# Kernel tuning notes

Hardware: AMD Instinct MI355X
Metric: run time of the kernel (lower is better)

The kernel has to match this reference:

```python
import jax, jax.numpy as jnp
import numpy as np

K, D, N, W, OUT = 16, 2, 16384, 256, 1
TW = 0.2  # fixed_transition_width


def setup_inputs() -> dict:
    key = jax.random.key(0)
    ks = jax.random.split(key, 9)
    # 4x4 grid of subdomains over [0,1]^2
    edges = np.linspace(0.0, 1.0, 5).astype(np.float32)
    mins = np.array([[edges[i], edges[j]] for i in range(4) for j in range(4)], np.float32)
    maxs = mins + 0.25

    def init_w(k, shape, fan_in):
        return jax.random.normal(k, shape, jnp.float32) / np.sqrt(fan_in).astype(np.float32)

    return {
        "x": jax.random.uniform(ks[0], (N, D), jnp.float32),
        "W0": init_w(ks[1], (K, D, W), D),
        "b0": jnp.zeros((K, W), jnp.float32),
        "W1": init_w(ks[2], (K, W, W), W),
        "b1": jnp.zeros((K, W), jnp.float32),
        "W2": init_w(ks[3], (K, W, W), W),
        "b2": jnp.zeros((K, W), jnp.float32),
        "W3": init_w(ks[4], (K, W, OUT), W),
        "b3": jnp.zeros((K, OUT), jnp.float32),
        "xmins": jnp.asarray(mins),
        "xmaxs": jnp.asarray(maxs),
    }


def _cosine_window(xmins, xmaxs, wmin, x):
    """Normalized cosine partition-of-unity weights. x:[N,D], xmins/xmaxs:[K,D] -> [N,K]."""
    # smooth ramp 0->1 over [xmin-w, xmin+w] and 1->0 over [xmax-w, xmax+w], per dim
    t_l = jnp.clip((x[None] - (xmins - wmin)[:, None]) / (2.0 * wmin), 0.0, 1.0)  # [K,N,D]
    t_r = jnp.clip(((xmaxs + wmin)[:, None] - x[None]) / (2.0 * wmin), 0.0, 1.0)
    w_raw = jnp.prod(0.25 * (1.0 - jnp.cos(jnp.pi * t_l)) * (1.0 - jnp.cos(jnp.pi * t_r)), axis=-1)  # [K,N]
    w = w_raw / (jnp.sum(w_raw, axis=0, keepdims=True) + 1e-9)
    return w.T  # [N,K]


def reference(x, W0, b0, W1, b1, W2, b2, W3, b3, xmins, xmaxs):
    all_w = _cosine_window(xmins, xmaxs, TW, x)  # [N,K]
    # per-subdomain normalization of x to [-1,1]
    center = (xmins + xmaxs) * 0.5
    scale = jnp.maximum((xmaxs - xmins) * 0.5, 1e-9)
    xn = (x[None] - center[:, None]) / scale[:, None]  # [K,N,D]
    # batched small MLPs (one per subdomain), tanh hidden activations
    h = jnp.tanh(jnp.einsum('knd,kdw->knw', xn, W0) + b0[:, None])
    h = jnp.tanh(jnp.einsum('knw,kwv->knv', h, W1) + b1[:, None])
    h = jnp.tanh(jnp.einsum('knw,kwv->knv', h, W2) + b2[:, None])
    sub = jnp.einsum('knw,kwo->kno', h, W3) + b3[:, None]  # [K,N,OUT]
    # window-weighted combine; ansatz is identity in the NN output
    return jnp.einsum('nk,kno->no', all_w, sub)  # [N,OUT]
```

## Files before the change

### kernel.cpp

```cpp
#include <hip/hip_runtime.h>
#include <stdint.h>

#define TWF 0.2f
#define NPTS 16384

typedef __attribute__((ext_vector_type(8))) short short8;
typedef __attribute__((ext_vector_type(4))) float floatx4;

__device__ __forceinline__ short f2bf(float f){
  unsigned u = __float_as_uint(f);
  u += 0x7fff + ((u >> 16) & 1);
  return (short)(u >> 16);
}
__device__ __forceinline__ float bf2f(short s){
  return __uint_as_float(((unsigned)(unsigned short)s) << 16);
}
__device__ __forceinline__ float fast_tanh(float x){
  float e = __builtin_amdgcn_exp2f(x * 2.885390082f);
  float r = __builtin_amdgcn_rcpf(e + 1.f);
  return fmaf(-2.f, r, 1.f);
}
__device__ __forceinline__ float cospi_t(float t){
  return __builtin_amdgcn_cosf(t * 0.5f);
}
__device__ __forceinline__ unsigned cvt_pk_bf16(float lo, float hi){
  unsigned r;
  asm("v_cvt_pk_bf16_f32 %0, %1, %2" : "=v"(r) : "v"(lo), "v"(hi));
  return r;
}

#define WS_W      0
#define WS_CNT    (4u<<20)
#define WS_ILIST  ((4u<<20) + 4096u)
#define WS_WLIST  ((5u<<20) + 4096u)
#define CNT(k)    counts[(k) * 32]

__global__ __launch_bounds__(256) void prep_fused(
    const float* __restrict__ W1, const float* __restrict__ W2,
    const float* __restrict__ x,  const float* __restrict__ xmins,
    const float* __restrict__ xmaxs, short* __restrict__ dst,
    int* __restrict__ counts, int* __restrict__ ilist, float* __restrict__ wlist,
    float* __restrict__ out){
  if (blockIdx.x < 1024){
    int gid = blockIdx.x * 256 + threadIdx.x;
    int lane = gid & 63; int rest = gid >> 6;
    int jt = rest & 15; rest >>= 4;
    int ks = rest & 7;  rest >>= 3;
    int k  = rest & 15; int mat = rest >> 4;
    const float* W = mat ? W2 : W1;
    int j   = jt * 16 + (lane & 15);
    int kk0 = ks * 32 + (lane >> 4) * 8;
    short8 v;
    #pragma unroll
    for (int jj = 0; jj < 8; jj++)
      v[jj] = f2bf(W[k * 65536 + (kk0 + jj) * 256 + j]);
    *(short8*)(dst + (size_t)gid * 8) = v;
  } else {
    __shared__ int s_wcnt[4];
    __shared__ int s_base;
    int b2    = blockIdx.x - 1024;
    int g     = b2 & 3;
    int chunk = b2 >> 2;
    int t     = threadIdx.x;
    int gid   = chunk * 256 + t;
    int lane  = t & 63, wave = t >> 6;
    if (g == 0) out[gid] = 0.f;
    float px = x[gid * 2 + 0], py = x[gid * 2 + 1];
    float wr[16]; float sum = 0.f;
    #pragma unroll
    for (int k = 0; k < 16; k++){
      float w = 1.f;
      #pragma unroll
      for (int d = 0; d < 2; d++){
        float xv = d ? py : px;
        float mn = xmins[k * 2 + d], mx = xmaxs[k * 2 + d];
        float tl = fminf(fmaxf((xv - (mn - TWF)) * (1.f / (2.f * TWF)), 0.f), 1.f);
        float tr = fminf(fmaxf(((mx + TWF) - xv) * (1.f / (2.f * TWF)), 0.f), 1.f);
        w *= 0.25f * (1.f - cospi_t(tl)) * (1.f - cospi_t(tr));
      }
      wr[k] = w; sum += w;
    }
    float inv = 1.f / (sum + 1e-9f);
    #pragma unroll 1
    for (int kk = 0; kk < 4; kk++){
      int k = g * 4 + ((kk + chunk) & 3);
      bool act = wr[k] > 0.f;
      unsigned long long mask = __ballot(act);
      if (lane == 0) s_wcnt[wave] = (int)__popcll(mask);
      __syncthreads();
      int tot = s_wcnt[0] + s_wcnt[1] + s_wcnt[2] + s_wcnt[3];
      int wpre = 0;
      #pragma unroll
      for (int w = 0; w < 4; w++) wpre += (w < wave) ? s_wcnt[w] : 0;
      if (t == 0) s_base = atomicAdd(&CNT(k), tot);
      __syncthreads();
      if (act){
        int pos = s_base + wpre + (int)__popcll(mask & ((1ull << lane) - 1ull));
        ilist[k * NPTS + pos] = gid;
        wlist[k * NPTS + pos] = wr[k] * inv;
      }
    }
  }
}

__device__ __forceinline__ void store_h_packed(
    short* lds_h, const floatx4 (&acc)[4][4], const floatx4 (&bb)[4],
    int wave, int quad, int col){
  #pragma unroll
  for (int rt = 0; rt < 4; rt++){
    const int j0    = (wave * 4 + rt) * 16 + quad * 4;
    const int cbase = j0 >> 3;
    const int off   = j0 & 7;
    #pragma unroll
    for (int ct = 0; ct < 4; ct++){
      const int m = ct * 16 + col;
      float t0 = fast_tanh(acc[rt][ct][0] + bb[rt][0]);
      float t1 = fast_tanh(acc[rt][ct][1] + bb[rt][1]);
      float t2 = fast_tanh(acc[rt][ct][2] + bb[rt][2]);
      float t3 = fast_tanh(acc[rt][ct][3] + bb[rt][3]);
      uint2 v = make_uint2(cvt_pk_bf16(t0, t1), cvt_pk_bf16(t2, t3));
      *(uint2*)&lds_h[m * 256 + ((cbase ^ (m & 7)) << 3) + off] = v;
    }
  }
}

__global__ __launch_bounds__(256, 4) void fbpinn_main(
    const float* __restrict__ x,  const float* __restrict__ W0, const float* __restrict__ b0,
    const float* __restrict__ b1, const float* __restrict__ b2,
    const float* __restrict__ W3, const float* __restrict__ b3,
    const float* __restrict__ xmins, const float* __restrict__ xmaxs,
    const short* __restrict__ wsw, const int* __restrict__ counts,
    const int* __restrict__ ilist, const float* __restrict__ wlist,
    float* __restrict__ out)
{
  __shared__ short lds_h[64 * 256];
  __shared__ float s_xn[64 * 2];
  __shared__ float s_win[64];
  __shared__ int   s_pidx[64];
  __shared__ float s_w3[256];
  __shared__ float s_w0[512];

  const int t    = threadIdx.x;
  const int lane = t & 63;
  const int wave = t >> 6;
  const int col  = lane & 15;
  const int quad = lane >> 4;

  int tb[17]; tb[0] = 0;
  #pragma unroll
  for (int kk = 0; kk < 16; kk++) tb[kk + 1] = tb[kk] + ((CNT(kk) + 63) >> 6);
  const int total = tb[16];

  const int xcd   = blockIdx.x & 7;
  const int nb    = gridDim.x >> 3;
  const int chunk = (total + 7) >> 3;

  for (int idx = blockIdx.x >> 3; idx < chunk; idx += nb){
    const int tile = xcd * chunk + idx;
    if (tile >= total) break;
    int k = 0;
    #pragma unroll
    for (int kk = 1; kk < 16; kk++) k += (tile >= tb[kk]);
    const int base = (tile - tb[k]) * 64;
    const int cnt  = CNT(k);

    __syncthreads();

    s_w3[t] = W3[k * 256 + t];
    s_w0[t] = W0[k * 512 + t];
    s_w0[256 + t] = W0[k * 512 + 256 + t];
    if (t < 64){
      int gi = base + t;
      bool valid = gi < cnt;
      int pidx = valid ? ilist[k * NPTS + gi] : 0;
      float w  = valid ? wlist[k * NPTS + gi] : 0.f;
      s_pidx[t] = pidx;
      s_win[t]  = w;
      float px = x[pidx * 2 + 0], py = x[pidx * 2 + 1];
      float cx = (xmins[k * 2 + 0] + xmaxs[k * 2 + 0]) * 0.5f;
      float cy = (xmins[k * 2 + 1] + xmaxs[k * 2 + 1]) * 0.5f;
      float sx = fmaxf((xmaxs[k * 2 + 0] - xmins[k * 2 + 0]) * 0.5f, 1e-9f);
      float sy = fmaxf((xmaxs[k * 2 + 1] - xmins[k * 2 + 1]) * 0.5f, 1e-9f);
      s_xn[t * 2 + 0] = (px - cx) / sx;
      s_xn[t * 2 + 1] = (py - cy) / sy;
    }
    __syncthreads();

    {
      short8 wfr[4], xfr[4];
      #pragma unroll
      for (int rt = 0; rt < 4; rt++){
        int j = (wave * 4 + rt) * 16 + col;
        short8 a;
        #pragma unroll
        for (int i = 0; i < 8; i++) a[i] = 0;
        a[0] = (quad == 0) ? f2bf(s_w0[j])       : (short)0;
        a[1] = (quad == 0) ? f2bf(s_w0[256 + j]) : (short)0;
        wfr[rt] = a;
      }
      #pragma unroll
      for (int ct = 0; ct < 4; ct++){
        int m = ct * 16 + col;
        short8 b;
        #pragma unroll
        for (int i = 0; i < 8; i++) b[i] = 0;
        b[0] = (quad == 0) ? f2bf(s_xn[m * 2 + 0]) : (short)0;
        b[1] = (quad == 0) ? f2bf(s_xn[m * 2 + 1]) : (short)0;
        xfr[ct] = b;
      }
      floatx4 bb[4];
      #pragma unroll
      for (int rt = 0; rt < 4; rt++)
        bb[rt] = *(const floatx4*)&b0[k * 256 + (wave * 4 + rt) * 16 + quad * 4];
      floatx4 acc[4][4];
      #pragma unroll
      for (int a = 0; a < 4; a++)
        #pragma unroll
        for (int b = 0; b < 4; b++)
          acc[a][b] = (floatx4){0.f, 0.f, 0.f, 0.f};
      #pragma unroll
      for (int rt = 0; rt < 4; rt++)
        #pragma unroll
        for (int ct = 0; ct < 4; ct++)
          acc[rt][ct] = __builtin_amdgcn_mfma_f32_16x16x32_bf16(wfr[rt], xfr[ct], acc[rt][ct], 0, 0, 0);
      store_h_packed(lds_h, acc, bb, wave, quad, col);
      __syncthreads();
    }

    #pragma unroll 1
    for (int layer = 0; layer < 2; layer++){
      const short8* wb = (const short8*)(wsw + (size_t)layer * 1048576)
                         + ((size_t)(k * 8) * 16 + wave * 4) * 64 + lane;
      const float*  bp = layer ? b2 : b1;
      floatx4 bb[4];
      #pragma unroll
      for (int rt = 0; rt < 4; rt++)
        bb[rt] = *(const floatx4*)&bp[k * 256 + (wave * 4 + rt) * 16 + quad * 4];
      floatx4 acc[4][4];
      #pragma unroll
      for (int a = 0; a < 4; a++)
        #pragma unroll
        for (int b = 0; b < 4; b++)
          acc[a][b] = (floatx4){0.f, 0.f, 0.f, 0.f};

      short8 wcur[4];
      #pragma unroll
      for (int rt = 0; rt < 4; rt++) wcur[rt] = wb[rt * 64];

      #pragma unroll
      for (int ks = 0; ks < 8; ks++){
        short8 wnxt[4];
        if (ks < 7){
          #pragma unroll
          for (int rt = 0; rt < 4; rt++)
            wnxt[rt] = wb[(ks + 1) * 1024 + rt * 64];
        }
        short8 hfr[4];
        #pragma unroll
        for (int ct = 0; ct < 4; ct++){
          int m   = ct * 16 + col;
          int pos = (ks * 4 + quad) ^ (m & 7);
          hfr[ct] = *(const short8*)&lds_h[m * 256 + pos * 8];
        }
        #pragma unroll
        for (int rt = 0; rt < 4; rt++)
          #pragma unroll
          for (int ct = 0; ct < 4; ct++)
            acc[rt][ct] = __builtin_amdgcn_mfma_f32_16x16x32_bf16(wcur[rt], hfr[ct], acc[rt][ct], 0, 0, 0);
        if (ks < 7){
          #pragma unroll
          for (int rt = 0; rt < 4; rt++) wcur[rt] = wnxt[rt];
        }
      }
      __syncthreads();

      store_h_packed(lds_h, acc, bb, wave, quad, col);
      __syncthreads();
    }

    {
      int m = t >> 2, q = t & 3;
      float dot = 0.f;
      #pragma unroll
      for (int cc = 0; cc < 8; cc++){
        int ci  = q * 8 + cc;
        int pos = ci ^ (m & 7);
        short8 hv = *(const short8*)&lds_h[m * 256 + pos * 8];
        #pragma unroll
        for (int jj = 0; jj < 8; jj++)
          dot = fmaf(bf2f(hv[jj]), s_w3[ci * 8 + jj], dot);
      }
      dot += __shfl_xor(dot, 1);
      dot += __shfl_xor(dot, 2);
      if (q == 0 && s_win[m] != 0.f)
        atomicAdd(&out[s_pidx[m]], s_win[m] * (dot + b3[k]));
    }
  }
}

extern "C" void kernel_launch(void* const* d_in, const int* in_sizes, int n_in,
                              void* d_out, int out_size, void* d_ws, size_t ws_size,
                              hipStream_t stream){
  const float* x     = (const float*)d_in[0];
  const float* W0    = (const float*)d_in[1];
  const float* b0    = (const float*)d_in[2];
  const float* W1    = (const float*)d_in[3];
  const float* b1    = (const float*)d_in[4];
  const float* W2    = (const float*)d_in[5];
  const float* b2    = (const float*)d_in[6];
  const float* W3    = (const float*)d_in[7];
  const float* b3    = (const float*)d_in[8];
  const float* xmins = (const float*)d_in[9];
  const float* xmaxs = (const float*)d_in[10];
  float* out = (float*)d_out;

  char* ws = (char*)d_ws;
  short* wsw   = (short*)(ws + WS_W);
  int*   cnts  = (int*)  (ws + WS_CNT);
  int*   ilist = (int*)  (ws + WS_ILIST);
  float* wlist = (float*)(ws + WS_WLIST);

  (void)hipMemsetAsync(cnts, 0, 4096, stream);
  prep_fused<<<1024 + 256, 256, 0, stream>>>(W1, W2, x, xmins, xmaxs,
                                             wsw, cnts, ilist, wlist, out);
  fbpinn_main<<<2048, 256, 0, stream>>>(x, W0, b0, b1, b2, W3, b3, xmins, xmaxs,
                                        wsw, cnts, ilist, wlist, out);
}
```

Baseline: 139.1 us.

## Pack point records in prep and reorganize bucketing per subdomain block

The bucketing part of the prep kernel now assigns each block one subdomain and 1024 points. It writes a single packed float4 record holding normalized coordinates, the normalized window weight and the point index, and needs only one atomic per block. The main kernel reads that record instead of gathering ilist, wlist and x and recomputing the normalization, which removes a dependent gather. The main grid is also halved to 1024 blocks. In exchange, each prep block recomputes all 16 window weights for four points per thread, and the record buffer is twice as large as before.

```diff
diff --git a/kernel.cpp b/kernel.cpp
--- a/kernel.cpp
+++ b/kernel.cpp
@@ -30,16 +30,15 @@
 }
 
 #define WS_W      0
-#define WS_CNT    (4u<<20)
-#define WS_ILIST  ((4u<<20) + 4096u)
-#define WS_WLIST  ((5u<<20) + 4096u)
+#define WS_REC    (4u<<20)
+#define WS_CNT    (8u<<20)
 #define CNT(k)    counts[(k) * 32]
 
 __global__ __launch_bounds__(256) void prep_fused(
     const float* __restrict__ W1, const float* __restrict__ W2,
     const float* __restrict__ x,  const float* __restrict__ xmins,
     const float* __restrict__ xmaxs, short* __restrict__ dst,
-    int* __restrict__ counts, int* __restrict__ ilist, float* __restrict__ wlist,
+    int* __restrict__ counts, floatx4* __restrict__ rec,
     float* __restrict__ out){
   if (blockIdx.x < 1024){
     int gid = blockIdx.x * 256 + threadIdx.x;
@@ -56,49 +55,80 @@
       v[jj] = f2bf(W[k * 65536 + (kk0 + jj) * 256 + j]);
     *(short8*)(dst + (size_t)gid * 8) = v;
   } else {
-    __shared__ int s_wcnt[4];
+    __shared__ int s_wrt[4][4];
     __shared__ int s_base;
-    int b2    = blockIdx.x - 1024;
-    int g     = b2 & 3;
-    int chunk = b2 >> 2;
-    int t     = threadIdx.x;
-    int gid   = chunk * 256 + t;
-    int lane  = t & 63, wave = t >> 6;
-    if (g == 0) out[gid] = 0.f;
-    float px = x[gid * 2 + 0], py = x[gid * 2 + 1];
-    float wr[16]; float sum = 0.f;
-    #pragma unroll
-    for (int k = 0; k < 16; k++){
-      float w = 1.f;
-      #pragma unroll
-      for (int d = 0; d < 2; d++){
-        float xv = d ? py : px;
-        float mn = xmins[k * 2 + d], mx = xmaxs[k * 2 + d];
-        float tl = fminf(fmaxf((xv - (mn - TWF)) * (1.f / (2.f * TWF)), 0.f), 1.f);
-        float tr = fminf(fmaxf(((mx + TWF) - xv) * (1.f / (2.f * TWF)), 0.f), 1.f);
-        w *= 0.25f * (1.f - cospi_t(tl)) * (1.f - cospi_t(tr));
-      }
-      wr[k] = w; sum += w;
-    }
-    float inv = 1.f / (sum + 1e-9f);
-    #pragma unroll 1
-    for (int kk = 0; kk < 4; kk++){
-      int k = g * 4 + ((kk + chunk) & 3);
-      bool act = wr[k] > 0.f;
-      unsigned long long mask = __ballot(act);
-      if (lane == 0) s_wcnt[wave] = (int)__popcll(mask);
-      __syncthreads();
-      int tot = s_wcnt[0] + s_wcnt[1] + s_wcnt[2] + s_wcnt[3];
-      int wpre = 0;
-      #pragma unroll
-      for (int w = 0; w < 4; w++) wpre += (w < wave) ? s_wcnt[w] : 0;
-      if (t == 0) s_base = atomicAdd(&CNT(k), tot);
-      __syncthreads();
-      if (act){
-        int pos = s_base + wpre + (int)__popcll(mask & ((1ull << lane) - 1ull));
-        ilist[k * NPTS + pos] = gid;
-        wlist[k * NPTS + pos] = wr[k] * inv;
-      }
+    int b2   = blockIdx.x - 1024;
+    int k    = b2 & 15;
+    int cb   = (b2 >> 4) * 1024;
+    int t    = threadIdx.x;
+    int lane = t & 63, wave = t >> 6;
+
+    float cx  = (xmins[k * 2 + 0] + xmaxs[k * 2 + 0]) * 0.5f;
+    float cy  = (xmins[k * 2 + 1] + xmaxs[k * 2 + 1]) * 0.5f;
+    float sxi = 1.f / fmaxf((xmaxs[k * 2 + 0] - xmins[k * 2 + 0]) * 0.5f, 1e-9f);
+    float syi = 1.f / fmaxf((xmaxs[k * 2 + 1] - xmins[k * 2 + 1]) * 0.5f, 1e-9f);
+
+    float pxr[4], pyr[4], sum[4], wk[4];
+    #pragma unroll
+    for (int r = 0; r < 4; r++){
+      int p = cb + r * 256 + t;
+      float2 xy = *(const float2*)&x[p * 2];
+      pxr[r] = xy.x; pyr[r] = xy.y; sum[r] = 0.f; wk[r] = 0.f;
+      if (k == 0) out[p] = 0.f;
+    }
+    #pragma unroll
+    for (int kk = 0; kk < 16; kk++){
+      float mnx = xmins[kk * 2 + 0], mny = xmins[kk * 2 + 1];
+      float mxx = xmaxs[kk * 2 + 0], mxy = xmaxs[kk * 2 + 1];
+      #pragma unroll
+      for (int r = 0; r < 4; r++){
+        float tlx = fminf(fmaxf((pxr[r] - (mnx - TWF)) * (1.f/(2.f*TWF)), 0.f), 1.f);
+        float trx = fminf(fmaxf(((mxx + TWF) - pxr[r]) * (1.f/(2.f*TWF)), 0.f), 1.f);
+        float tly = fminf(fmaxf((pyr[r] - (mny - TWF)) * (1.f/(2.f*TWF)), 0.f), 1.f);
+        float tr2 = fminf(fmaxf(((mxy + TWF) - pyr[r]) * (1.f/(2.f*TWF)), 0.f), 1.f);
+        float wx = 0.25f * (1.f - cospi_t(tlx)) * (1.f - cospi_t(trx));
+        float wy = 0.25f * (1.f - cospi_t(tly)) * (1.f - cospi_t(tr2));
+        float w  = wx * wy;
+        sum[r] += w;
+        if (kk == k) wk[r] = w;
+      }
+    }
+    bool act[4]; float wn[4], xa[4], xb[4];
+    unsigned long long msk[4]; int wtot[4];
+    #pragma unroll
+    for (int r = 0; r < 4; r++){
+      float inv = 1.f / (sum[r] + 1e-9f);
+      act[r] = wk[r] > 0.f;
+      wn[r]  = wk[r] * inv;
+      xa[r]  = (pxr[r] - cx) * sxi;
+      xb[r]  = (pyr[r] - cy) * syi;
+      msk[r] = __ballot(act[r]);
+      wtot[r] = (int)__popcll(msk[r]);
+    }
+    if (lane == 0){
+      #pragma unroll
+      for (int r = 0; r < 4; r++) s_wrt[wave][r] = wtot[r];
+    }
+    __syncthreads();
+    int wavebase = 0, blocktot = 0;
+    #pragma unroll
+    for (int w = 0; w < 4; w++){
+      int ws_ = s_wrt[w][0] + s_wrt[w][1] + s_wrt[w][2] + s_wrt[w][3];
+      blocktot += ws_;
+      wavebase += (w < wave) ? ws_ : 0;
+    }
+    if (t == 0) s_base = atomicAdd(&CNT(k), blocktot);
+    __syncthreads();
+    int rb = 0;
+    #pragma unroll
+    for (int r = 0; r < 4; r++){
+      if (act[r]){
+        int pos = s_base + wavebase + rb +
+                  (int)__popcll(msk[r] & ((1ull << lane) - 1ull));
+        int p = cb + r * 256 + t;
+        rec[k * NPTS + pos] = (floatx4){xa[r], xb[r], wn[r], __int_as_float(p)};
+      }
+      rb += s_wrt[wave][r];
     }
   }
 }
@@ -125,13 +155,11 @@
 }
 
 __global__ __launch_bounds__(256, 4) void fbpinn_main(
-    const float* __restrict__ x,  const float* __restrict__ W0, const float* __restrict__ b0,
+    const float* __restrict__ W0, const float* __restrict__ b0,
     const float* __restrict__ b1, const float* __restrict__ b2,
     const float* __restrict__ W3, const float* __restrict__ b3,
-    const float* __restrict__ xmins, const float* __restrict__ xmaxs,
     const short* __restrict__ wsw, const int* __restrict__ counts,
-    const int* __restrict__ ilist, const float* __restrict__ wlist,
-    float* __restrict__ out)
+    const floatx4* __restrict__ rec, float* __restrict__ out)
 {
   __shared__ short lds_h[64 * 256];
   __shared__ float s_xn[64 * 2];
@@ -172,17 +200,11 @@
     if (t < 64){
       int gi = base + t;
       bool valid = gi < cnt;
-      int pidx = valid ? ilist[k * NPTS + gi] : 0;
-      float w  = valid ? wlist[k * NPTS + gi] : 0.f;
-      s_pidx[t] = pidx;
-      s_win[t]  = w;
-      float px = x[pidx * 2 + 0], py = x[pidx * 2 + 1];
-      float cx = (xmins[k * 2 + 0] + xmaxs[k * 2 + 0]) * 0.5f;
-      float cy = (xmins[k * 2 + 1] + xmaxs[k * 2 + 1]) * 0.5f;
-      float sx = fmaxf((xmaxs[k * 2 + 0] - xmins[k * 2 + 0]) * 0.5f, 1e-9f);
-      float sy = fmaxf((xmaxs[k * 2 + 1] - xmins[k * 2 + 1]) * 0.5f, 1e-9f);
-      s_xn[t * 2 + 0] = (px - cx) / sx;
-      s_xn[t * 2 + 1] = (py - cy) / sy;
+      floatx4 rc = rec[k * NPTS + (valid ? gi : 0)];
+      s_pidx[t] = __float_as_int(rc[3]);
+      s_win[t]  = valid ? rc[2] : 0.f;
+      s_xn[t * 2 + 0] = rc[0];
+      s_xn[t * 2 + 1] = rc[1];
     }
     __syncthreads();
 
@@ -315,14 +337,13 @@
   float* out = (float*)d_out;
 
   char* ws = (char*)d_ws;
-  short* wsw   = (short*)(ws + WS_W);
-  int*   cnts  = (int*)  (ws + WS_CNT);
-  int*   ilist = (int*)  (ws + WS_ILIST);
-  float* wlist = (float*)(ws + WS_WLIST);
+  short*   wsw  = (short*)  (ws + WS_W);
+  floatx4* rc   = (floatx4*)(ws + WS_REC);
+  int*     cnts = (int*)    (ws + WS_CNT);
 
   (void)hipMemsetAsync(cnts, 0, 4096, stream);
   prep_fused<<<1024 + 256, 256, 0, stream>>>(W1, W2, x, xmins, xmaxs,
-                                             wsw, cnts, ilist, wlist, out);
-  fbpinn_main<<<2048, 256, 0, stream>>>(x, W0, b0, b1, b2, W3, b3, xmins, xmaxs,
-                                        wsw, cnts, ilist, wlist, out);
-}
+                                             wsw, cnts, rc, out);
+  fbpinn_main<<<1024, 256, 0, stream>>>(W0, b0, b1, b2, W3, b3,
+                                        wsw, cnts, rc, out);
+}
```

After: 148.1 us. +6.5%, slower.
